# Kernel tuning notes

Measured on AMD Instinct MI355X. Metric: run time of the kernel, lower is better.

Reference implementation:

```python
import jax, jax.numpy as jnp
import numpy as np

B, S, D_IN, H = 64, 1024, 1024, 1024


def setup_inputs() -> dict:
    key = jax.random.key(0)
    ks = jax.random.split(key, 5)
    scale_x = 1.0 / np.sqrt(D_IN)
    scale_h = 1.0 / np.sqrt(H)
    # gate order along leading axis: f, i, o, g
    W = jax.random.uniform(ks[0], (4, D_IN, H), jnp.float32, -scale_x, scale_x)
    bW = jax.random.uniform(ks[1], (4, H), jnp.float32, -scale_x, scale_x)
    U = jax.random.uniform(ks[2], (4, H, H), jnp.float32, -scale_h, scale_h)
    bU = jax.random.uniform(ks[3], (4, H), jnp.float32, -scale_h, scale_h)
    input_emb = jax.random.normal(ks[4], (B, S, D_IN), jnp.float32)
    return {"input_emb": input_emb, "W": W, "bW": bW, "U": U, "bU": bU}


def reference(input_emb, W, bW, U, bU):
    b, s, _ = input_emb.shape
    h_dim = W.shape[-1]
    # Precompute input projections for all 4 gates across all timesteps: (S, B, 4, H)
    xproj = jnp.einsum('bsd,kdh->sbkh', input_emb, W) + bW

    def step(carry, xt):
        h_prev, c_prev = carry
        # recurrent projection for all gates: (B, 4, H)
        gates = xt + jnp.einsum('bh,kho->bko', h_prev, U) + bU
        f_t = jax.nn.sigmoid(gates[:, 0])
        i_t = jax.nn.sigmoid(gates[:, 1])
        o_t = jax.nn.sigmoid(gates[:, 2])
        g_t = jax.nn.sigmoid(gates[:, 3])  # NOTE: original uses sigmoid here, not tanh
        c_t = f_t * c_prev + i_t * g_t
        h_t = o_t * jnp.tanh(c_t)
        return (h_t, c_t), h_t

    h0 = jnp.zeros((b, h_dim), input_emb.dtype)
    c0 = jnp.zeros((b, h_dim), input_emb.dtype)
    (h_last, c_last), ys = jax.lax.scan(step, (h0, c0), xproj)
    outputs = jnp.transpose(ys, (1, 0, 2))  # (B, S, H)
    return outputs, (h_last, c_last)
```

## Files before the change

### kernel.cpp

```cpp
#include <hip/hip_runtime.h>
#include <hip/hip_bf16.h>
#include <stdint.h>


typedef __attribute__((ext_vector_type(8))) short short8;
typedef __attribute__((ext_vector_type(4))) float floatx4;
typedef __attribute__((ext_vector_type(2))) float floatx2;

__device__ __forceinline__ unsigned short f2bf(float x){
  union { float f; unsigned int u; } v; v.f = x;
  unsigned int r = v.u + 0x7fffu + ((v.u >> 16) & 1u);
  return (unsigned short)(r >> 16);
}
__device__ __forceinline__ float bf2f(unsigned short b){
  union { unsigned int u; float f; } v; v.u = ((unsigned int)b) << 16; return v.f;
}
__device__ __forceinline__ float fsigmoid(float x){ return 1.0f / (1.0f + __expf(-x)); }
__device__ __forceinline__ float ftanh(float x){ return 1.0f - 2.0f / (1.0f + __expf(2.0f * x)); }

__global__ void k_transpose_bf16(const float* __restrict__ src, unsigned short* __restrict__ dst){
  __shared__ float tile[64][65];
  const int g  = blockIdx.z;
  const int d0 = blockIdx.x * 64;
  const int h0 = blockIdx.y * 64;
  const int t  = threadIdx.x;
  const float* s    = src + ((size_t)g << 20);
  unsigned short* o = dst + ((size_t)g << 20);
  #pragma unroll
  for (int i = 0; i < 16; i++){
    int e = i * 256 + t;
    int r = e >> 6, c = e & 63;
    tile[r][c] = s[(size_t)(d0 + r) * 1024 + (h0 + c)];
  }
  __syncthreads();
  #pragma unroll
  for (int i = 0; i < 16; i++){
    int e = i * 256 + t;
    int a = e >> 6, bb = e & 63;
    o[(size_t)(h0 + a) * 1024 + (d0 + bb)] = f2bf(tile[bb][a]);
  }
}

__global__ void k_convert_x(const float* __restrict__ inp, unsigned short* __restrict__ abuf, int s0){
  int idx = blockIdx.x * 256 + threadIdx.x;
  int e = idx * 4;
  int r = e >> 10, d = e & 1023;
  int b = r & 63, sl = r >> 6;
  floatx4 v = *(const floatx4*)(inp + ((size_t)(b * 1024 + (s0 + sl)) * 1024 + d));
  unsigned long long pk = (unsigned long long)f2bf(v[0])
                        | ((unsigned long long)f2bf(v[1]) << 16)
                        | ((unsigned long long)f2bf(v[2]) << 32)
                        | ((unsigned long long)f2bf(v[3]) << 48);
  *(unsigned long long*)(abuf + (size_t)r * 1024 + d) = pk;
}

__global__ void __launch_bounds__(256) k_gemm_xproj(
    const unsigned short* __restrict__ A,
    const unsigned short* __restrict__ Bt,
    const float* __restrict__ bW,
    const float* __restrict__ bU,
    unsigned short* __restrict__ Cc)
{
  __shared__ unsigned short As[2][128][64];
  __shared__ unsigned short Bs[2][128][64];
  const int t = threadIdx.x;
  const int w = t >> 6;
  const int lane = t & 63;
  const int m0 = blockIdx.x * 128;
  const int n0 = blockIdx.y * 128;
  floatx4 acc[4][4];
  #pragma unroll
  for (int i = 0; i < 4; i++)
    #pragma unroll
    for (int j = 0; j < 4; j++)
      acc[i][j] = (floatx4){0.f, 0.f, 0.f, 0.f};

  auto stage = [&](int bufi, int kt){
    #pragma unroll
    for (int i = 0; i < 4; i++){
      int chunk = i * 256 + t;
      int r = chunk >> 3, j = chunk & 7;
      int js = j ^ (r & 7);
      __builtin_amdgcn_global_load_lds(
        (const __attribute__((address_space(1))) unsigned int*)(A + (size_t)(m0 + r) * 1024 + kt * 64 + js * 8),
        (__attribute__((address_space(3))) unsigned int*)(&As[bufi][0][0] + (i * 256 + w * 64) * 8), 16, 0, 0);
    }
    #pragma unroll
    for (int i = 0; i < 4; i++){
      int chunk = i * 256 + t;
      int r = chunk >> 3, j = chunk & 7;
      int js = j ^ (r & 7);
      __builtin_amdgcn_global_load_lds(
        (const __attribute__((address_space(1))) unsigned int*)(Bt + (size_t)(n0 + r) * 1024 + kt * 64 + js * 8),
        (__attribute__((address_space(3))) unsigned int*)(&Bs[bufi][0][0] + (i * 256 + w * 64) * 8), 16, 0, 0);
    }
  };

  auto compute = [&](int bufi){
    const int mi0 = (w >> 1) * 64;
    const int ni0 = (w & 1) * 64;
    #pragma unroll
    for (int kc = 0; kc < 2; kc++){
      short8 af[4], bfr[4];
      #pragma unroll
      for (int mi = 0; mi < 4; mi++){
        int row = mi0 + mi * 16 + (lane & 15);
        int j = kc * 4 + (lane >> 4);
        af[mi] = *(const short8*)&As[bufi][row][(j ^ (row & 7)) * 8];
      }
      #pragma unroll
      for (int ni = 0; ni < 4; ni++){
        int row = ni0 + ni * 16 + (lane & 15);
        int j = kc * 4 + (lane >> 4);
        bfr[ni] = *(const short8*)&Bs[bufi][row][(j ^ (row & 7)) * 8];
      }
      #pragma unroll
      for (int mi = 0; mi < 4; mi++)
        #pragma unroll
        for (int ni = 0; ni < 4; ni++)
          acc[mi][ni] = __builtin_amdgcn_mfma_f32_16x16x32_bf16(af[mi], bfr[ni], acc[mi][ni], 0, 0, 0);
    }
  };

  stage(0, 0);
  int buf = 0;
  for (int kt = 0; kt < 16; kt++){
    __syncthreads();
    if (kt < 15) stage(buf ^ 1, kt + 1);
    compute(buf);
    buf ^= 1;
  }

  {
    const int mi0 = (w >> 1) * 64;
    const int ni0 = (w & 1) * 64;
    #pragma unroll
    for (int ni = 0; ni < 4; ni++){
      int col = n0 + ni0 + ni * 16 + (lane & 15);
      float bias = bW[col] + bU[col];
      #pragma unroll
      for (int mi = 0; mi < 4; mi++){
        int mrow = m0 + mi0 + mi * 16 + (lane >> 4) * 4;
        #pragma unroll
        for (int r = 0; r < 4; r++)
          Cc[(size_t)(mrow + r) * 4096 + col] = f2bf(acc[mi][ni][r] + bias);
      }
    }
  }
}

__global__ void __launch_bounds__(256, 1) k_lstm_rec(
    const unsigned short* __restrict__ xp,
    const unsigned short* __restrict__ Ut,
    unsigned short* hbs,
    float* cstate,
    float* __restrict__ out,
    float* __restrict__ hlast,
    float* __restrict__ clast,
    int* flags,
    int s_base, int SC)
{
  const int t = threadIdx.x;
  const int w = t >> 6;
  const int lane = t & 63;
  const int wgid = blockIdx.x;
  const int g  = wgid & 3;
  const int j  = wgid >> 2;
  const int B0 = g * 16;
  const int gc0 = j * 32;

  __shared__ float glds[4][16][33];

  short8 bfrag0[32], bfrag1[32];
  {
    const unsigned short* bp0 = Ut + (size_t)(w * 1024 + gc0 + (lane & 15)) * 1024 + (lane >> 4) * 8;
    const unsigned short* bp1 = bp0 + (size_t)16 * 1024;
    #pragma unroll
    for (int kc = 0; kc < 32; kc++){
      bfrag0[kc] = *(const short8*)(bp0 + kc * 32);
      bfrag1[kc] = *(const short8*)(bp1 + kc * 32);
    }
  }

  const int b   = t >> 4;
  const int cc2 = (t & 15) * 2;
  floatx2 cst;
  if (s_base == 0) cst = (floatx2){0.f, 0.f};
  else             cst = *(const floatx2*)&cstate[(size_t)(B0 + b) * 1024 + gc0 + cc2];

  int bail = 20000000;
  const int fb = g * 32;

  for (int sl = 0; sl < SC; sl++){
    const int s = s_base + sl;
    const int p = s & 1;

    unsigned int xu[4];
    {
      const unsigned short* xr = xp + ((size_t)(sl * 64 + B0 + b)) * 4096 + gc0 + cc2;
      #pragma unroll
      for (int gg = 0; gg < 4; gg++) xu[gg] = *(const unsigned int*)(xr + gg * 1024);
    }
    __builtin_amdgcn_sched_barrier(0);

    const char* gsrc = (const char*)hbs + ((size_t)p * 4 + g) * 32768;
    floatx4 acc0 = (floatx4){0.f,0.f,0.f,0.f};
    floatx4 acc1 = (floatx4){0.f,0.f,0.f,0.f};

    auto wait_chunk = [&](int c){
      if (s == 0) return;
      const int* fp2 = &flags[fb + c * 8 + (lane & 7)];
      while (true){
        int v = __hip_atomic_load(fp2, __ATOMIC_RELAXED, __HIP_MEMORY_SCOPE_AGENT);
        if (__all(v >= s)) break;
        __builtin_amdgcn_s_sleep(1);
        if (--bail < 0) break;
      }
    };

    unsigned long long loA[8], hiA[8], loB[8], hiB[8];
    auto issue8 = [&](unsigned long long (&lo)[8], unsigned long long (&hi)[8], int ch){
      #pragma unroll
      for (int i = 0; i < 8; i++){
        const unsigned long long* sp2 = (const unsigned long long*)(gsrc + (ch * 8 + i) * 1024 + lane * 16);
        lo[i] = __hip_atomic_load(sp2,     __ATOMIC_RELAXED, __HIP_MEMORY_SCOPE_AGENT);
        hi[i] = __hip_atomic_load(sp2 + 1, __ATOMIC_RELAXED, __HIP_MEMORY_SCOPE_AGENT);
      }
    };
    auto crunch8 = [&](unsigned long long (&lo)[8], unsigned long long (&hi)[8], int ch){
      #pragma unroll
      for (int i = 0; i < 8; i++){
        union { unsigned long long q[2]; short8 v; } u;
        u.q[0] = lo[i]; u.q[1] = hi[i];
        asm volatile("s_nop 1\n\tv_mfma_f32_16x16x32_bf16 %0, %1, %2, %0"
                     : "+v"(acc0) : "v"(u.v), "a"(bfrag0[ch * 8 + i]));
        asm volatile("v_mfma_f32_16x16x32_bf16 %0, %1, %2, %0"
                     : "+v"(acc1) : "v"(u.v), "a"(bfrag1[ch * 8 + i]));
      }
    };
    wait_chunk(0);
    issue8(loA, hiA, 0);
    wait_chunk(1);
    issue8(loB, hiB, 1);
    crunch8(loA, hiA, 0);
    wait_chunk(2);
    issue8(loA, hiA, 2);
    crunch8(loB, hiB, 1);
    wait_chunk(3);
    issue8(loB, hiB, 3);
    crunch8(loA, hiA, 2);
    crunch8(loB, hiB, 3);
    asm volatile("s_nop 7\n\ts_nop 7\n\ts_nop 7" ::: "memory");

    {
      const int r0 = (lane >> 4) * 4;
      const int cl = lane & 15;
      #pragma unroll
      for (int r = 0; r < 4; r++){
        glds[w][r0 + r][cl]      = acc0[r];
        glds[w][r0 + r][16 + cl] = acc1[r];
      }
    }
    __syncthreads();

    float hout[2];
    #pragma unroll
    for (int d = 0; d < 2; d++){
      float fv = fsigmoid(glds[0][b][cc2 + d] + bf2f((unsigned short)(xu[0] >> (16 * d))));
      float iv = fsigmoid(glds[1][b][cc2 + d] + bf2f((unsigned short)(xu[1] >> (16 * d))));
      float ov = fsigmoid(glds[2][b][cc2 + d] + bf2f((unsigned short)(xu[2] >> (16 * d))));
      float gv = fsigmoid(glds[3][b][cc2 + d] + bf2f((unsigned short)(xu[3] >> (16 * d))));
      float cv = fv * cst[d] + iv * gv;
      cst[d] = cv;
      hout[d] = ov * ftanh(cv);
    }

    {
      unsigned int hv = (unsigned int)f2bf(hout[0]) | ((unsigned int)f2bf(hout[1]) << 16);
      unsigned int* dst = (unsigned int*)((char*)hbs + ((size_t)(p ^ 1) * 4 + g) * 32768 + j * 1024
                + (((cc2 >> 3) * 16 + b) << 4) + ((cc2 & 7) << 1));
      __hip_atomic_store(dst, hv, __ATOMIC_RELAXED, __HIP_MEMORY_SCOPE_AGENT);
    }

    if (s == 1023){
      *(floatx2*)&hlast[(size_t)(B0 + b) * 1024 + gc0 + cc2] = (floatx2){hout[0], hout[1]};
      *(floatx2*)&clast[(size_t)(B0 + b) * 1024 + gc0 + cc2] = cst;
    }

    asm volatile("s_waitcnt vmcnt(0)" ::: "memory");
    __syncthreads();
    if (t == 0)
      __hip_atomic_store(&flags[fb + j], s + 1, __ATOMIC_RELAXED, __HIP_MEMORY_SCOPE_AGENT);

    *(floatx2*)&out[((size_t)(B0 + b) * 1024 + s) * 1024 + gc0 + cc2] = (floatx2){hout[0], hout[1]};
  }

  *(floatx2*)&cstate[(size_t)(B0 + b) * 1024 + gc0 + cc2] = cst;
}

extern "C" void kernel_launch(void* const* d_in, const int* in_sizes, int n_in,
                              void* d_out, int out_size, void* d_ws, size_t ws_size,
                              hipStream_t stream)
{
  (void)in_sizes; (void)n_in; (void)out_size;
  const float* input_emb = (const float*)d_in[0];
  const float* W   = (const float*)d_in[1];
  const float* bWp = (const float*)d_in[2];
  const float* U   = (const float*)d_in[3];
  const float* bUp = (const float*)d_in[4];
  float* out   = (float*)d_out;
  float* hlast = out + (size_t)64 * 1024 * 1024;
  float* clast = hlast + 64 * 1024;

  char* base = (char*)d_ws;
  unsigned short* Wt  = (unsigned short*)base;  base += 8388608;
  unsigned short* Ut  = (unsigned short*)base;  base += 8388608;
  unsigned short* hbs = (unsigned short*)base;  base += 262144;
  float* cstate       = (float*)base;           base += 262144;
  int* flags          = (int*)base;             base += 8192;
  size_t fixed = (size_t)(base - (char*)d_ws);
  size_t avail = ws_size > fixed ? ws_size - fixed : 0;
  int SC = 1024;
  while (SC > 8 && (size_t)SC * 655360ull > avail) SC >>= 1;
  unsigned short* Abuf = (unsigned short*)base; base += (size_t)SC * 131072;
  unsigned short* xpb  = (unsigned short*)base;

  hipMemsetAsync(flags, 0, 8192, stream);
  hipMemsetAsync(hbs, 0, 262144, stream);

  k_transpose_bf16<<<dim3(16, 16, 4), 256, 0, stream>>>(W, Wt);
  k_transpose_bf16<<<dim3(16, 16, 4), 256, 0, stream>>>(U, Ut);

  int nch = 1024 / SC;
  for (int cc = 0; cc < nch; cc++){
    int s0 = cc * SC;
    k_convert_x<<<SC * 64, 256, 0, stream>>>(input_emb, Abuf, s0);
    k_gemm_xproj<<<dim3(SC / 2, 32), 256, 0, stream>>>(Abuf, Wt, bWp, bUp, xpb);
    k_lstm_rec<<<128, 256, 0, stream>>>(xpb, Ut, hbs, cstate, out, hlast, clast, flags, s0, SC);
  }
}
```

Before: 5.998 ms.

## Fuse input-projection GEMM with LSTM recurrence via producer-consumer workgroups

Merges the xproj GEMM and the recurrent LSTM kernel into one launch of 256 workgroups. 128 workgroups run as persistent GEMM producers that walk the M tiles in timestep order and bump per-tile counters in global memory. The other 128 run the recurrence and spin on those counters before reading each pair of timesteps. This overlaps the large input-projection GEMM with the latency-bound recurrence, so the recurrence no longer waits for the whole GEMM to finish. The cost is that the GEMM now runs on only 128 workgroups, and the design assumes all 256 workgroups are resident at once, otherwise the spin-waits could deadlock.

Result: faster. 5.278 ms (median of 2 runs) (-12.0%).

```diff
diff --git a/kernel.cpp b/kernel.cpp
--- a/kernel.cpp
+++ b/kernel.cpp
@@ -54,103 +54,12 @@
   *(unsigned long long*)(abuf + (size_t)r * 1024 + d) = pk;
 }
 
-__global__ void __launch_bounds__(256) k_gemm_xproj(
-    const unsigned short* __restrict__ A,
-    const unsigned short* __restrict__ Bt,
+__global__ void __launch_bounds__(256, 1) k_fused(
+    const unsigned short* __restrict__ Abuf,
+    const unsigned short* __restrict__ Wt,
     const float* __restrict__ bW,
     const float* __restrict__ bU,
-    unsigned short* __restrict__ Cc)
-{
-  __shared__ unsigned short As[2][128][64];
-  __shared__ unsigned short Bs[2][128][64];
-  const int t = threadIdx.x;
-  const int w = t >> 6;
-  const int lane = t & 63;
-  const int m0 = blockIdx.x * 128;
-  const int n0 = blockIdx.y * 128;
-  floatx4 acc[4][4];
-  #pragma unroll
-  for (int i = 0; i < 4; i++)
-    #pragma unroll
-    for (int j = 0; j < 4; j++)
-      acc[i][j] = (floatx4){0.f, 0.f, 0.f, 0.f};
-
-  auto stage = [&](int bufi, int kt){
-    #pragma unroll
-    for (int i = 0; i < 4; i++){
-      int chunk = i * 256 + t;
-      int r = chunk >> 3, j = chunk & 7;
-      int js = j ^ (r & 7);
-      __builtin_amdgcn_global_load_lds(
-        (const __attribute__((address_space(1))) unsigned int*)(A + (size_t)(m0 + r) * 1024 + kt * 64 + js * 8),
-        (__attribute__((address_space(3))) unsigned int*)(&As[bufi][0][0] + (i * 256 + w * 64) * 8), 16, 0, 0);
-    }
-    #pragma unroll
-    for (int i = 0; i < 4; i++){
-      int chunk = i * 256 + t;
-      int r = chunk >> 3, j = chunk & 7;
-      int js = j ^ (r & 7);
-      __builtin_amdgcn_global_load_lds(
-        (const __attribute__((address_space(1))) unsigned int*)(Bt + (size_t)(n0 + r) * 1024 + kt * 64 + js * 8),
-        (__attribute__((address_space(3))) unsigned int*)(&Bs[bufi][0][0] + (i * 256 + w * 64) * 8), 16, 0, 0);
-    }
-  };
-
-  auto compute = [&](int bufi){
-    const int mi0 = (w >> 1) * 64;
-    const int ni0 = (w & 1) * 64;
-    #pragma unroll
-    for (int kc = 0; kc < 2; kc++){
-      short8 af[4], bfr[4];
-      #pragma unroll
-      for (int mi = 0; mi < 4; mi++){
-        int row = mi0 + mi * 16 + (lane & 15);
-        int j = kc * 4 + (lane >> 4);
-        af[mi] = *(const short8*)&As[bufi][row][(j ^ (row & 7)) * 8];
-      }
-      #pragma unroll
-      for (int ni = 0; ni < 4; ni++){
-        int row = ni0 + ni * 16 + (lane & 15);
-        int j = kc * 4 + (lane >> 4);
-        bfr[ni] = *(const short8*)&Bs[bufi][row][(j ^ (row & 7)) * 8];
-      }
-      #pragma unroll
-      for (int mi = 0; mi < 4; mi++)
-        #pragma unroll
-        for (int ni = 0; ni < 4; ni++)
-          acc[mi][ni] = __builtin_amdgcn_mfma_f32_16x16x32_bf16(af[mi], bfr[ni], acc[mi][ni], 0, 0, 0);
-    }
-  };
-
-  stage(0, 0);
-  int buf = 0;
-  for (int kt = 0; kt < 16; kt++){
-    __syncthreads();
-    if (kt < 15) stage(buf ^ 1, kt + 1);
-    compute(buf);
-    buf ^= 1;
-  }
-
-  {
-    const int mi0 = (w >> 1) * 64;
-    const int ni0 = (w & 1) * 64;
-    #pragma unroll
-    for (int ni = 0; ni < 4; ni++){
-      int col = n0 + ni0 + ni * 16 + (lane & 15);
-      float bias = bW[col] + bU[col];
-      #pragma unroll
-      for (int mi = 0; mi < 4; mi++){
-        int mrow = m0 + mi0 + mi * 16 + (lane >> 4) * 4;
-        #pragma unroll
-        for (int r = 0; r < 4; r++)
-          Cc[(size_t)(mrow + r) * 4096 + col] = f2bf(acc[mi][ni][r] + bias);
-      }
-    }
-  }
-}
-
-__global__ void __launch_bounds__(256, 1) k_lstm_rec(
-    const unsigned short* __restrict__ xp,
+    unsigned short* __restrict__ xp,
     const unsigned short* __restrict__ Ut,
     unsigned short* hbs,
     float* cstate,
@@ -158,18 +67,125 @@
     float* __restrict__ hlast,
     float* __restrict__ clast,
     int* flags,
+    int* mcnt,
     int s_base, int SC)
 {
+  union Smem {
+    struct { unsigned short As[2][128][64]; unsigned short Bs[2][128][64]; } g;
+    float glds[4][16][33];
+  };
+  __shared__ Smem sm;
+
   const int t = threadIdx.x;
+
+  if (blockIdx.x < 128){
+    const int pwg = blockIdx.x;
+    const int w = t >> 6;
+    const int lane = t & 63;
+    const int ntiles = SC * 16;
+
+    for (int tile = pwg; tile < ntiles; tile += 128){
+      const int mt = tile >> 5, nt = tile & 31;
+      const int m0 = mt * 128, n0 = nt * 128;
+
+      floatx4 acc[4][4];
+      #pragma unroll
+      for (int i = 0; i < 4; i++)
+        #pragma unroll
+        for (int jj = 0; jj < 4; jj++)
+          acc[i][jj] = (floatx4){0.f, 0.f, 0.f, 0.f};
+
+      auto stage = [&](int bufi, int kt){
+        #pragma unroll
+        for (int i = 0; i < 4; i++){
+          int chunk = i * 256 + t;
+          int r = chunk >> 3, jx = chunk & 7;
+          int js = jx ^ (r & 7);
+          __builtin_amdgcn_global_load_lds(
+            (const __attribute__((address_space(1))) unsigned int*)(Abuf + (size_t)(m0 + r) * 1024 + kt * 64 + js * 8),
+            (__attribute__((address_space(3))) unsigned int*)(&sm.g.As[bufi][0][0] + (i * 256 + w * 64) * 8), 16, 0, 0);
+        }
+        #pragma unroll
+        for (int i = 0; i < 4; i++){
+          int chunk = i * 256 + t;
+          int r = chunk >> 3, jx = chunk & 7;
+          int js = jx ^ (r & 7);
+          __builtin_amdgcn_global_load_lds(
+            (const __attribute__((address_space(1))) unsigned int*)(Wt + (size_t)(n0 + r) * 1024 + kt * 64 + js * 8),
+            (__attribute__((address_space(3))) unsigned int*)(&sm.g.Bs[bufi][0][0] + (i * 256 + w * 64) * 8), 16, 0, 0);
+        }
+      };
+
+      auto compute = [&](int bufi){
+        const int mi0 = (w >> 1) * 64;
+        const int ni0 = (w & 1) * 64;
+        #pragma unroll
+        for (int kc = 0; kc < 2; kc++){
+          short8 af[4], bfr[4];
+          #pragma unroll
+          for (int mi = 0; mi < 4; mi++){
+            int row = mi0 + mi * 16 + (lane & 15);
+            int jx = kc * 4 + (lane >> 4);
+            af[mi] = *(const short8*)&sm.g.As[bufi][row][(jx ^ (row & 7)) * 8];
+          }
+          #pragma unroll
+          for (int ni = 0; ni < 4; ni++){
+            int row = ni0 + ni * 16 + (lane & 15);
+            int jx = kc * 4 + (lane >> 4);
+            bfr[ni] = *(const short8*)&sm.g.Bs[bufi][row][(jx ^ (row & 7)) * 8];
+          }
+          #pragma unroll
+          for (int mi = 0; mi < 4; mi++)
+            #pragma unroll
+            for (int ni = 0; ni < 4; ni++)
+              acc[mi][ni] = __builtin_amdgcn_mfma_f32_16x16x32_bf16(af[mi], bfr[ni], acc[mi][ni], 0, 0, 0);
+        }
+      };
+
+      stage(0, 0);
+      int buf = 0;
+      for (int kt = 0; kt < 16; kt++){
+        __syncthreads();
+        if (kt < 15) stage(buf ^ 1, kt + 1);
+        compute(buf);
+        buf ^= 1;
+      }
+
+      {
+        const int mi0 = (w >> 1) * 64;
+        const int ni0 = (w & 1) * 64;
+        #pragma unroll
+        for (int ni = 0; ni < 4; ni++){
+          int col = n0 + ni0 + ni * 16 + (lane & 15);
+          float bias = bW[col] + bU[col];
+          #pragma unroll
+          for (int mi = 0; mi < 4; mi++){
+            int mrow = m0 + mi0 + mi * 16 + (lane >> 4) * 4;
+            #pragma unroll
+            for (int r = 0; r < 4; r++)
+              xp[(size_t)(mrow + r) * 4096 + col] = f2bf(acc[mi][ni][r] + bias);
+          }
+        }
+      }
+
+      asm volatile("s_waitcnt vmcnt(0)" ::: "memory");
+      __syncthreads();
+      if (t == 0){
+        __builtin_amdgcn_fence(__ATOMIC_RELEASE, "agent");
+        __hip_atomic_fetch_add(&mcnt[mt], 1, __ATOMIC_RELAXED, __HIP_MEMORY_SCOPE_AGENT);
+      }
+      __syncthreads();
+    }
+    return;
+  }
+
   const int w = t >> 6;
   const int lane = t & 63;
-  const int wgid = blockIdx.x;
+  const int wgid = blockIdx.x - 128;
   const int g  = wgid & 3;
   const int j  = wgid >> 2;
   const int B0 = g * 16;
   const int gc0 = j * 32;
-
-  __shared__ float glds[4][16][33];
 
   short8 bfrag0[32], bfrag1[32];
   {
@@ -194,6 +210,17 @@
   for (int sl = 0; sl < SC; sl++){
     const int s = s_base + sl;
     const int p = s & 1;
+
+    if (!(sl & 1)){
+      const int mt = sl >> 1;
+      while (true){
+        int v = __hip_atomic_load(&mcnt[mt], __ATOMIC_RELAXED, __HIP_MEMORY_SCOPE_AGENT);
+        if (__all(v >= 32)) break;
+        __builtin_amdgcn_s_sleep(2);
+        if (--bail < 0) break;
+      }
+      asm volatile("" ::: "memory");
+    }
 
     unsigned int xu[4];
     {
@@ -257,8 +284,8 @@
       const int cl = lane & 15;
       #pragma unroll
       for (int r = 0; r < 4; r++){
-        glds[w][r0 + r][cl]      = acc0[r];
-        glds[w][r0 + r][16 + cl] = acc1[r];
+        sm.glds[w][r0 + r][cl]      = acc0[r];
+        sm.glds[w][r0 + r][16 + cl] = acc1[r];
       }
     }
     __syncthreads();
@@ -266,10 +293,10 @@
     float hout[2];
     #pragma unroll
     for (int d = 0; d < 2; d++){
-      float fv = fsigmoid(glds[0][b][cc2 + d] + bf2f((unsigned short)(xu[0] >> (16 * d))));
-      float iv = fsigmoid(glds[1][b][cc2 + d] + bf2f((unsigned short)(xu[1] >> (16 * d))));
-      float ov = fsigmoid(glds[2][b][cc2 + d] + bf2f((unsigned short)(xu[2] >> (16 * d))));
-      float gv = fsigmoid(glds[3][b][cc2 + d] + bf2f((unsigned short)(xu[3] >> (16 * d))));
+      float fv = fsigmoid(sm.glds[0][b][cc2 + d] + bf2f((unsigned short)(xu[0] >> (16 * d))));
+      float iv = fsigmoid(sm.glds[1][b][cc2 + d] + bf2f((unsigned short)(xu[1] >> (16 * d))));
+      float ov = fsigmoid(sm.glds[2][b][cc2 + d] + bf2f((unsigned short)(xu[2] >> (16 * d))));
+      float gv = fsigmoid(sm.glds[3][b][cc2 + d] + bf2f((unsigned short)(xu[3] >> (16 * d))));
       float cv = fv * cst[d] + iv * gv;
       cst[d] = cv;
       hout[d] = ov * ftanh(cv);
@@ -318,6 +345,7 @@
   unsigned short* hbs = (unsigned short*)base;  base += 262144;
   float* cstate       = (float*)base;           base += 262144;
   int* flags          = (int*)base;             base += 8192;
+  int* mcnt           = (int*)base;             base += 4096;
   size_t fixed = (size_t)(base - (char*)d_ws);
   size_t avail = ws_size > fixed ? ws_size - fixed : 0;
   int SC = 1024;
@@ -334,8 +362,9 @@
   int nch = 1024 / SC;
   for (int cc = 0; cc < nch; cc++){
     int s0 = cc * SC;
+    hipMemsetAsync(mcnt, 0, 4096, stream);
     k_convert_x<<<SC * 64, 256, 0, stream>>>(input_emb, Abuf, s0);
-    k_gemm_xproj<<<dim3(SC / 2, 32), 256, 0, stream>>>(Abuf, Wt, bWp, bUp, xpb);
-    k_lstm_rec<<<128, 256, 0, stream>>>(xpb, Ut, hbs, cstate, out, hlast, clast, flags, s0, SC);
-  }
-}
+    k_fused<<<256, 256, 0, stream>>>(Abuf, Wt, bWp, bUp, xpb, Ut, hbs, cstate,
+                                     out, hlast, clast, flags, mcnt, s0, SC);
+  }
+}
```
